# Kernel tuning notes

Hardware: AMD Instinct MI355X
Metric: run time of the kernel (lower is better)

## Reference

```python
import jax, jax.numpy as jnp
import numpy as np

B, L, S = 4, 512, 100
NG, GS = 19, 5          # 19 clades of 5 species; species 95..99 are singleton clades
VOCAB = 6
HID = 512
HPOOL = 4               # num_attention_heads // 2
D = 64                  # hidden_size / num_attention_heads
ALL = HPOOL * D         # 256
FIRE_H = 32
TIME_SCALE = 1.0        # from time_enc = 'fire_1'
MAX_DIST = 20.0         # config.max_evol_dist


def setup_inputs() -> dict:
    key = jax.random.key(0)
    ks = jax.random.split(key, 10)
    return {
        "source_ids": jax.random.randint(ks[0], (B, L, S), 0, VOCAB, dtype=jnp.int32),
        "in_clade_phylo_dist": jax.random.uniform(ks[1], (S,), dtype=jnp.float32) * MAX_DIST,
        "attn_w_emb": jax.random.normal(ks[2], (VOCAB, HPOOL), dtype=jnp.float32) * 0.02,
        "value_emb": jax.random.normal(ks[3], (VOCAB, ALL), dtype=jnp.float32) * 0.02,
        "ffn_w": jax.random.normal(ks[4], (ALL, HID), dtype=jnp.float32) * 0.02,
        "ffn_b": jnp.zeros((HID,), dtype=jnp.float32),
        "embed_tab": jax.random.normal(ks[5], (VOCAB, HID), dtype=jnp.float32) * 0.02,
        "fire_c": jnp.float32(100.0),
        "fire_w1": jax.random.normal(ks[6], (FIRE_H,), dtype=jnp.float32) * 0.5,
        "fire_w2": jax.random.normal(ks[7], (FIRE_H,), dtype=jnp.float32) * 0.5,
    }


def reference(source_ids, in_clade_phylo_dist, attn_w_emb, value_emb,
              ffn_w, ffn_b, embed_tab, fire_c, fire_w1, fire_w2):
    # --- FIRE time bias: scalar MLP per species distance -> bias[s] ---
    c = jnp.maximum(fire_c, 0.0)
    rel = in_clade_phylo_dist * TIME_SCALE                      # [S]
    rel = jnp.log(c * rel + 1.0) / jnp.log(c * MAX_DIST + 1.0)  # [S]
    h = jax.nn.silu(rel[:, None] * fire_w1[None, :])            # [S, FIRE_H]
    bias = h @ fire_w2                                          # [S]

    # --- multi-species clades: embedding-based attention pooling ---
    grp = jnp.arange(NG * GS).reshape(NG, GS)                   # static clade layout
    ids_g = source_ids[..., :NG * GS].reshape(B, L, NG, GS)     # [B,L,NG,GS]
    scores = jnp.swapaxes(attn_w_emb[ids_g], -1, -2)            # [B,L,NG,H,GS]
    scores = scores + bias[grp][None, None, :, None, :]
    probs = jax.nn.softmax(scores, axis=-1)                     # dropout p=0 (eval)
    vals = value_emb[ids_g].reshape(B, L, NG, GS, HPOOL, D)     # [B,L,NG,GS,H,D]
    pooled = jnp.einsum('blnhg,blnghd->blnhd', probs, vals)     # [B,L,NG,H,D]
    pooled = pooled.reshape(B, L, NG, ALL)
    pooled = pooled @ ffn_w + ffn_b                             # [B,L,NG,HID]

    # --- singleton clades: plain embedding lookup ---
    singles = embed_tab[source_ids[..., NG * GS:]]              # [B,L,5,HID]

    return jnp.concatenate([pooled, singles], axis=-2)          # [B,L,24,HID]
```

## Files before the change

### kernel.cpp

```cpp
#include <hip/hip_runtime.h>

#define B_      4
#define L_      512
#define S_      100
#define NG_     19
#define GS_     5
#define VOCAB_  6
#define HID_    512
#define HPOOL_  4
#define D_      64
#define ALL_    256
#define FIREH_  32
#define MAXDIST_ 20.0f


__global__ __launch_bounds__(128) void prep_kernel(
    const float* __restrict__ dist,
    const float* __restrict__ value_emb,
    const float* __restrict__ ffn_w,
    const float* __restrict__ fire_c,
    const float* __restrict__ fire_w1,
    const float* __restrict__ fire_w2,
    float* __restrict__ bias_out,
    float* __restrict__ W2_out)
{
  const int b = blockIdx.x;
  const int t = threadIdx.x;
  if (b < VOCAB_ * HPOOL_ * 4) {
    const int q   = b >> 2;
    const int col = (b & 3) * 128 + t;
    const int v = q >> 2;
    const int h = q & 3;
    float acc = 0.f;
#pragma unroll
    for (int k = 0; k < D_; ++k) {
      acc = fmaf(value_emb[v * ALL_ + h * D_ + k],
                 ffn_w[(h * D_ + k) * HID_ + col], acc);
    }
    W2_out[q * HID_ + col] = acc;
  } else {
    if (t < S_) {
      const float c = fmaxf(fire_c[0], 0.f);
      const float denom = logf(fmaf(c, MAXDIST_, 1.f));
      const float rel = logf(fmaf(c, dist[t], 1.f)) / denom;
      float acc = 0.f;
#pragma unroll
      for (int i = 0; i < FIREH_; ++i) {
        const float x = rel * fire_w1[i];
        const float s = x / (1.f + expf(-x));
        acc = fmaf(s, fire_w2[i], acc);
      }
      bias_out[t] = acc;
    }
  }
}

__global__ __launch_bounds__(256) void main_kernel(
    const int*   __restrict__ ids,
    const float* __restrict__ attn_w,
    const float* __restrict__ embed_tab,
    const float* __restrict__ ffn_b,
    const float* __restrict__ bias,
    const float* __restrict__ W2,
    float* __restrict__ out)
{
  const int bl = blockIdx.x;
  const int t  = threadIdx.x;

  __shared__ int s_ids[S_];
  __shared__ float s_bias[S_];
  __shared__ float s_aw[VOCAB_ * HPOOL_];
  __shared__ __align__(16) float s_cw[NG_][24];

  if (t < S_) s_ids[t] = ids[bl * S_ + t];
  else if (t >= 100 && t < 200) s_bias[t - 100] = bias[t - 100];
  else if (t >= 224 && t < 248) s_aw[t - 224] = attn_w[t - 224];
#pragma unroll
  for (int i = t; i < NG_ * 24; i += 256) ((float*)s_cw)[i] = 0.f;
  __syncthreads();

  if (t < NG_ * HPOOL_) {
    const int n = t >> 2;
    const int h = t & 3;
    int   idg[GS_];
    float p[GS_];
    float m = -1e30f;
#pragma unroll
    for (int g = 0; g < GS_; ++g) {
      idg[g] = s_ids[n * GS_ + g];
      p[g] = s_aw[idg[g] * HPOOL_ + h] + s_bias[n * GS_ + g];
      m = fmaxf(m, p[g]);
    }
    float s = 0.f;
#pragma unroll
    for (int g = 0; g < GS_; ++g) { p[g] = expf(p[g] - m); s += p[g]; }
    const float inv = 1.f / s;
#pragma unroll
    for (int g = 0; g < GS_; ++g) {
      s_cw[n][idg[g] * HPOOL_ + h] += p[g] * inv;
    }
  }
  __syncthreads();

  float2 w2r[24];
#pragma unroll
  for (int q = 0; q < 24; ++q)
    w2r[q] = *(const float2*)&W2[q * HID_ + 2 * t];
  const float2 bb = *(const float2*)&ffn_b[2 * t];

  float* op = out + (size_t)bl * 24 * HID_ + 2 * t;

  for (int n = 0; n < NG_; ++n) {
    float2 acc = bb;
    const float4* cw4 = (const float4*)s_cw[n];
#pragma unroll
    for (int q4 = 0; q4 < 6; ++q4) {
      const float4 c = cw4[q4];
      acc.x = fmaf(c.x, w2r[q4 * 4 + 0].x, acc.x);
      acc.y = fmaf(c.x, w2r[q4 * 4 + 0].y, acc.y);
      acc.x = fmaf(c.y, w2r[q4 * 4 + 1].x, acc.x);
      acc.y = fmaf(c.y, w2r[q4 * 4 + 1].y, acc.y);
      acc.x = fmaf(c.z, w2r[q4 * 4 + 2].x, acc.x);
      acc.y = fmaf(c.z, w2r[q4 * 4 + 2].y, acc.y);
      acc.x = fmaf(c.w, w2r[q4 * 4 + 3].x, acc.x);
      acc.y = fmaf(c.w, w2r[q4 * 4 + 3].y, acc.y);
    }
    *(float2*)(op + n * HID_) = acc;
  }

#pragma unroll
  for (int j = 0; j < 5; ++j) {
    const int id = s_ids[NG_ * GS_ + j];
    *(float2*)(op + (NG_ + j) * HID_) =
        *(const float2*)&embed_tab[id * HID_ + 2 * t];
  }
}

extern "C" void kernel_launch(void* const* d_in, const int* in_sizes, int n_in,
                              void* d_out, int out_size, void* d_ws, size_t ws_size,
                              hipStream_t stream) {
  const int*   src_ids = (const int*)  d_in[0];
  const float* dist    = (const float*)d_in[1];
  const float* attn_w  = (const float*)d_in[2];
  const float* valemb  = (const float*)d_in[3];
  const float* ffn_w   = (const float*)d_in[4];
  const float* ffn_b   = (const float*)d_in[5];
  const float* emb_tab = (const float*)d_in[6];
  const float* fire_c  = (const float*)d_in[7];
  const float* fire_w1 = (const float*)d_in[8];
  const float* fire_w2 = (const float*)d_in[9];

  float* out  = (float*)d_out;
  float* ws   = (float*)d_ws;
  float* bias = ws;
  float* W2   = ws + 128;

  hipLaunchKernelGGL(prep_kernel, dim3(97), dim3(128), 0, stream,
                     dist, valemb, ffn_w, fire_c, fire_w1, fire_w2, bias, W2);
  hipLaunchKernelGGL(main_kernel, dim3(B_ * L_), dim3(256), 0, stream,
                     src_ids, attn_w, emb_tab, ffn_b, bias, W2, out);
}
```

Before: 31.47 us.

## Hoist W2 loads before softmax barrier, split accumulators, fast exp, occupancy hint

The per-thread W2 and bias register loads now start before the first barrier, so their latency can overlap the shared-memory setup and the softmax phase. The singleton embedding copies are issued before the pooled projection loop. The projection now uses four independent accumulator chains instead of one to shorten the FMA dependency chain, and expf is replaced by __expf. A min-blocks-per-CU hint of 6 is added to launch_bounds, which may cap registers, and the fast exp and reordered summation slightly change numerics.

```diff
diff --git a/kernel.cpp b/kernel.cpp
--- a/kernel.cpp
+++ b/kernel.cpp
@@ -13,6 +13,10 @@
 #define FIREH_  32
 #define MAXDIST_ 20.0f
 
+typedef float f32x2 __attribute__((ext_vector_type(2)));
+typedef float f32x4 __attribute__((ext_vector_type(4)));
+
+#define NROWS_  (B_ * L_)
 
 __global__ __launch_bounds__(128) void prep_kernel(
     const float* __restrict__ dist,
@@ -29,33 +33,38 @@
   if (b < VOCAB_ * HPOOL_ * 4) {
     const int q   = b >> 2;
     const int col = (b & 3) * 128 + t;
-    const int v = q >> 2;
-    const int h = q & 3;
+    const int v = q >> 2, h = q & 3;
     float acc = 0.f;
 #pragma unroll
-    for (int k = 0; k < D_; ++k) {
+    for (int k = 0; k < D_; ++k)
       acc = fmaf(value_emb[v * ALL_ + h * D_ + k],
                  ffn_w[(h * D_ + k) * HID_ + col], acc);
+    W2_out[q * HID_ + col] = acc;
+  } else if (t < S_) {
+    const float c = fmaxf(fire_c[0], 0.f);
+    const float denom = logf(fmaf(c, MAXDIST_, 1.f));
+    const float rel = logf(fmaf(c, dist[t], 1.f)) / denom;
+    float acc = 0.f;
+#pragma unroll
+    for (int i = 0; i < FIREH_; ++i) {
+      const float x = rel * fire_w1[i];
+      acc = fmaf(x / (1.f + __expf(-x)), fire_w2[i], acc);
     }
-    W2_out[q * HID_ + col] = acc;
-  } else {
-    if (t < S_) {
-      const float c = fmaxf(fire_c[0], 0.f);
-      const float denom = logf(fmaf(c, MAXDIST_, 1.f));
-      const float rel = logf(fmaf(c, dist[t], 1.f)) / denom;
-      float acc = 0.f;
-#pragma unroll
-      for (int i = 0; i < FIREH_; ++i) {
-        const float x = rel * fire_w1[i];
-        const float s = x / (1.f + expf(-x));
-        acc = fmaf(s, fire_w2[i], acc);
-      }
-      bias_out[t] = acc;
-    }
+    bias_out[t] = acc;
   }
 }
 
-__global__ __launch_bounds__(256) void main_kernel(
+#define QB(C, BASE)                                                    \
+  a0.x = fmaf(C.x, w2r[BASE + 0].x, a0.x);                             \
+  a0.y = fmaf(C.x, w2r[BASE + 0].y, a0.y);                             \
+  a1.x = fmaf(C.y, w2r[BASE + 1].x, a1.x);                             \
+  a1.y = fmaf(C.y, w2r[BASE + 1].y, a1.y);                             \
+  a2.x = fmaf(C.z, w2r[BASE + 2].x, a2.x);                             \
+  a2.y = fmaf(C.z, w2r[BASE + 2].y, a2.y);                             \
+  a3.x = fmaf(C.w, w2r[BASE + 3].x, a3.x);                             \
+  a3.y = fmaf(C.w, w2r[BASE + 3].y, a3.y);
+
+__global__ __launch_bounds__(256, 6) void main_kernel(
     const int*   __restrict__ ids,
     const float* __restrict__ attn_w,
     const float* __restrict__ embed_tab,
@@ -67,7 +76,7 @@
   const int bl = blockIdx.x;
   const int t  = threadIdx.x;
 
-  __shared__ int s_ids[S_];
+  __shared__ int   s_ids[S_];
   __shared__ float s_bias[S_];
   __shared__ float s_aw[VOCAB_ * HPOOL_];
   __shared__ __align__(16) float s_cw[NG_][24];
@@ -75,16 +84,20 @@
   if (t < S_) s_ids[t] = ids[bl * S_ + t];
   else if (t >= 100 && t < 200) s_bias[t - 100] = bias[t - 100];
   else if (t >= 224 && t < 248) s_aw[t - 224] = attn_w[t - 224];
+
+  f32x2 w2r[24];
+#pragma unroll
+  for (int q = 0; q < 24; ++q)
+    w2r[q] = *(const f32x2*)&W2[q * HID_ + 2 * t];
+  const f32x2 bb = *(const f32x2*)&ffn_b[2 * t];
+
 #pragma unroll
   for (int i = t; i < NG_ * 24; i += 256) ((float*)s_cw)[i] = 0.f;
   __syncthreads();
 
   if (t < NG_ * HPOOL_) {
-    const int n = t >> 2;
-    const int h = t & 3;
-    int   idg[GS_];
-    float p[GS_];
-    float m = -1e30f;
+    const int n = t >> 2, h = t & 3;
+    int idg[GS_]; float p[GS_]; float m = -1e30f;
 #pragma unroll
     for (int g = 0; g < GS_; ++g) {
       idg[g] = s_ids[n * GS_ + g];
@@ -93,46 +106,34 @@
     }
     float s = 0.f;
 #pragma unroll
-    for (int g = 0; g < GS_; ++g) { p[g] = expf(p[g] - m); s += p[g]; }
+    for (int g = 0; g < GS_; ++g) { p[g] = __expf(p[g] - m); s += p[g]; }
     const float inv = 1.f / s;
 #pragma unroll
-    for (int g = 0; g < GS_; ++g) {
+    for (int g = 0; g < GS_; ++g)
       s_cw[n][idg[g] * HPOOL_ + h] += p[g] * inv;
-    }
   }
   __syncthreads();
 
-  float2 w2r[24];
-#pragma unroll
-  for (int q = 0; q < 24; ++q)
-    w2r[q] = *(const float2*)&W2[q * HID_ + 2 * t];
-  const float2 bb = *(const float2*)&ffn_b[2 * t];
-
   float* op = out + (size_t)bl * 24 * HID_ + 2 * t;
-
-  for (int n = 0; n < NG_; ++n) {
-    float2 acc = bb;
-    const float4* cw4 = (const float4*)s_cw[n];
-#pragma unroll
-    for (int q4 = 0; q4 < 6; ++q4) {
-      const float4 c = cw4[q4];
-      acc.x = fmaf(c.x, w2r[q4 * 4 + 0].x, acc.x);
-      acc.y = fmaf(c.x, w2r[q4 * 4 + 0].y, acc.y);
-      acc.x = fmaf(c.y, w2r[q4 * 4 + 1].x, acc.x);
-      acc.y = fmaf(c.y, w2r[q4 * 4 + 1].y, acc.y);
-      acc.x = fmaf(c.z, w2r[q4 * 4 + 2].x, acc.x);
-      acc.y = fmaf(c.z, w2r[q4 * 4 + 2].y, acc.y);
-      acc.x = fmaf(c.w, w2r[q4 * 4 + 3].x, acc.x);
-      acc.y = fmaf(c.w, w2r[q4 * 4 + 3].y, acc.y);
-    }
-    *(float2*)(op + n * HID_) = acc;
-  }
 
 #pragma unroll
   for (int j = 0; j < 5; ++j) {
     const int id = s_ids[NG_ * GS_ + j];
-    *(float2*)(op + (NG_ + j) * HID_) =
-        *(const float2*)&embed_tab[id * HID_ + 2 * t];
+    *(f32x2*)(op + (NG_ + j) * HID_) =
+        *(const f32x2*)&embed_tab[id * HID_ + 2 * t];
+  }
+
+  for (int n = 0; n < NG_; ++n) {
+    const f32x4* cw4 = (const f32x4*)s_cw[n];
+    const f32x4 c0 = cw4[0], c1 = cw4[1], c2 = cw4[2],
+                c3 = cw4[3], c4 = cw4[4], c5 = cw4[5];
+    f32x2 a0 = bb;
+    f32x2 a1 = {0.f, 0.f}, a2 = {0.f, 0.f}, a3 = {0.f, 0.f};
+    QB(c0, 0) QB(c1, 4) QB(c2, 8) QB(c3, 12) QB(c4, 16) QB(c5, 20)
+    f32x2 acc;
+    acc.x = (a0.x + a1.x) + (a2.x + a3.x);
+    acc.y = (a0.y + a1.y) + (a2.y + a3.y);
+    *(f32x2*)(op + n * HID_) = acc;
   }
 }
 
@@ -157,6 +158,6 @@
 
   hipLaunchKernelGGL(prep_kernel, dim3(97), dim3(128), 0, stream,
                      dist, valemb, ffn_w, fire_c, fire_w1, fire_w2, bias, W2);
-  hipLaunchKernelGGL(main_kernel, dim3(B_ * L_), dim3(256), 0, stream,
+  hipLaunchKernelGGL(main_kernel, dim3(NROWS_), dim3(256), 0, stream,
                      src_ids, attn_w, emb_tab, ffn_b, bias, W2, out);
 }
```

Result: slower. 32.17 us (+2.2%).
